# Kernel tuning notes

Measured on AMD Instinct MI355X. Metric: run time of the kernel, lower is better.

Reference implementation:

```python
import jax, jax.numpy as jnp
import numpy as np

TOP_K = 2
CAP_FACTOR = 1.25
MIN_CAPACITY = 4


def setup_inputs() -> dict:
    key = jax.random.key(0)
    k1, k2, k3, k4 = jax.random.split(key, 4)
    B, T, C, E = 8, 2048, 1024, 8
    x = jax.random.normal(k1, (B, T, C), dtype=jnp.float32)
    w_g = jax.random.normal(k2, (E, C), dtype=jnp.float32) * 0.02   # router gate (Linear, no bias)
    c_fc = jax.random.normal(k3, (E, C, 4 * C), dtype=jnp.float32) * 0.02
    c_proj = jax.random.normal(k4, (E, 4 * C, C), dtype=jnp.float32) * 0.02
    return {"x": x, "w_g": w_g, "c_fc": c_fc, "c_proj": c_proj}


def reference(x, w_g, c_fc, c_proj):
    B, T, C = x.shape
    E = w_g.shape[0]
    N = B * T
    capacity = max(MIN_CAPACITY, int(CAP_FACTOR * N * TOP_K / E))  # 5120, static

    xf = x.reshape(N, C)
    # ---- Router (eval path: no noise, no aux losses) ----
    logits = xf @ w_g.T                                   # [N, E]
    top_logits, top_idx = jax.lax.top_k(logits, TOP_K)    # [N, k]
    router_probs = jax.nn.softmax(top_logits, axis=-1)    # [N, k]

    # position in expert: cumsum over (k-major, token) flattened order
    oh = jax.nn.one_hot(top_idx, E, dtype=jnp.int32)      # [N, k, E]
    oh_t = oh.transpose(1, 0, 2).reshape(TOP_K * N, E)
    pos = jnp.cumsum(oh_t, axis=0).reshape(TOP_K, N, E).transpose(1, 0, 2)  # [N, k, E]
    rank = jnp.sum((pos - 1) * oh, axis=-1)               # [N, k], 0-based slot in expert buffer
    valid = rank < capacity                               # capacity mask
    probs_masked = router_probs * valid.astype(router_probs.dtype)
    rank_c = jnp.clip(rank, 0, capacity - 1)

    # ---- Dispatch: scatter tokens into [E, capacity, C] buffers ----
    contrib = xf[:, None, :] * valid[..., None].astype(xf.dtype)  # [N, k, C]
    buf = jnp.zeros((E, capacity, C), dtype=xf.dtype).at[top_idx, rank_c].add(contrib)

    # ---- Experts: bmm -> ReLU^2 -> bmm ----
    h = jnp.einsum('ecd,edf->ecf', buf, c_fc)             # [E, cap, 4C]
    h = jnp.square(jax.nn.relu(h))
    expert_out = jnp.einsum('ecf,efd->ecd', h, c_proj)    # [E, cap, C]

    # ---- Combine: gather expert outputs back, weight by router probs ----
    gathered = expert_out[top_idx, rank_c]                # [N, k, C]
    out = jnp.sum(gathered * probs_masked[..., None], axis=1)
    return out.reshape(B, T, C)
```

## Files before the change

### kernel.cpp

```cpp
#include <hip/hip_runtime.h>

#define NE 8
#define CAP 5120
#define NT 16384
#define CD 1024
#define FCD 4096

typedef __attribute__((ext_vector_type(8))) short short8;
typedef __attribute__((ext_vector_type(4))) float f32x4;

__device__ __forceinline__ unsigned short f2bf(float f) {
  unsigned int u = __builtin_bit_cast(unsigned int, f);
  u += 0x7FFFu + ((u >> 16) & 1u);
  return (unsigned short)(u >> 16);
}
__device__ __forceinline__ float bf2f(unsigned short u) {
  unsigned int v = ((unsigned int)u) << 16;
  return __builtin_bit_cast(float, v);
}
__device__ __forceinline__ void g2lds16(const unsigned short* g, unsigned short* l) {
  __builtin_amdgcn_global_load_lds(
      (const __attribute__((address_space(1))) unsigned int*)(unsigned long long)g,
      (__attribute__((address_space(3))) unsigned int*)l,
      16, 0, 0);
}

__global__ __launch_bounds__(256) void fill_i32_k(int* __restrict__ p, int v, int n) {
  int i = blockIdx.x * 256 + threadIdx.x;
  if (i < n) p[i] = v;
}
__global__ __launch_bounds__(256) void fill_zero_f32x4_k(float4* __restrict__ p, size_t n4) {
  size_t i = (size_t)blockIdx.x * 256 + threadIdx.x;
  if (i < n4) p[i] = make_float4(0.f, 0.f, 0.f, 0.f);
}

__global__ __launch_bounds__(256) void transpose_bf16_k(
    const float* __restrict__ in, unsigned short* __restrict__ out, int R, int Cc) {
  __shared__ float tile[64][65];
  const size_t esz = (size_t)R * Cc;
  const float* inp = in + (size_t)blockIdx.z * esz;
  unsigned short* outp = out + (size_t)blockIdx.z * esz;
  const int cbase = blockIdx.x * 64, rbase = blockIdx.y * 64;
  const int t = threadIdx.x;
#pragma unroll
  for (int i = 0; i < 4; ++i) {
    int idx = i * 256 + t;
    int r = idx >> 4, c4 = (idx & 15) * 4;
    const float4 v = *reinterpret_cast<const float4*>(inp + (size_t)(rbase + r) * Cc + cbase + c4);
    tile[r][c4 + 0] = v.x; tile[r][c4 + 1] = v.y; tile[r][c4 + 2] = v.z; tile[r][c4 + 3] = v.w;
  }
  __syncthreads();
#pragma unroll
  for (int i = 0; i < 4; ++i) {
    int idx = i * 256 + t;
    int oc = idx >> 4, q = (idx & 15) * 4;
    ushort4 o;
    o.x = f2bf(tile[q + 0][oc]); o.y = f2bf(tile[q + 1][oc]);
    o.z = f2bf(tile[q + 2][oc]); o.w = f2bf(tile[q + 3][oc]);
    *reinterpret_cast<ushort4*>(outp + (size_t)(cbase + oc) * R + rbase + q) = o;
  }
}

__global__ __launch_bounds__(256) void router_k(
    const float* __restrict__ x, const float* __restrict__ wg,
    unsigned short* __restrict__ xb, int* __restrict__ topidx, float* __restrict__ probs) {
  __shared__ float wls[NE * CD];
  const int t = threadIdx.x;
  {
    const float4* w4 = (const float4*)wg;
    float4* l4 = (float4*)wls;
    for (int i = t; i < NE * CD / 4; i += 256) l4[i] = w4[i];
  }
  __syncthreads();
  const int wave = t >> 6, lane = t & 63;
  const int gw = blockIdx.x * 4 + wave;
  const float4* wls4 = (const float4*)wls;
#pragma unroll
  for (int it = 0; it < 2; ++it) {
    const int n = gw * 2 + it;
    const float4* xr4 = (const float4*)(x + (size_t)n * CD);
    ushort4* xb4 = (ushort4*)(xb + (size_t)n * CD);
    double acc[NE] = {0, 0, 0, 0, 0, 0, 0, 0};
#pragma unroll
    for (int j = 0; j < 4; ++j) {
      const int idx = j * 64 + lane;
      const float4 xv = xr4[idx];
      ushort4 o;
      o.x = f2bf(xv.x); o.y = f2bf(xv.y); o.z = f2bf(xv.z); o.w = f2bf(xv.w);
      xb4[idx] = o;
#pragma unroll
      for (int e = 0; e < NE; ++e) {
        const float4 wv = wls4[e * 256 + idx];
        acc[e] += (double)xv.x * (double)wv.x + (double)xv.y * (double)wv.y
                + (double)xv.z * (double)wv.z + (double)xv.w * (double)wv.w;
      }
    }
#pragma unroll
    for (int s = 32; s >= 1; s >>= 1) {
#pragma unroll
      for (int e = 0; e < NE; ++e) acc[e] += __shfl_xor(acc[e], s, 64);
    }
    if (lane == 0) {
      int i1 = 0; double v1 = acc[0];
      for (int e = 1; e < NE; ++e) if (acc[e] > v1) { v1 = acc[e]; i1 = e; }
      int i2 = -1; double v2 = -1e300;
      for (int e = 0; e < NE; ++e) if (e != i1 && acc[e] > v2) { v2 = acc[e]; i2 = e; }
      float p0 = 1.0f / (1.0f + expf((float)(v2 - v1)));
      topidx[n * 2 + 0] = i1; topidx[n * 2 + 1] = i2;
      probs[n * 2 + 0] = p0; probs[n * 2 + 1] = 1.0f - p0;
    }
  }
}

__global__ __launch_bounds__(256) void hist_k(const int* __restrict__ topidx, int* __restrict__ blkhist) {
  __shared__ int h[16];
  const int t = threadIdx.x;
  if (t < 16) h[t] = 0;
  __syncthreads();
  const int n = blockIdx.x * 256 + t;
  atomicAdd(&h[topidx[n * 2 + 0]], 1);
  atomicAdd(&h[8 + topidx[n * 2 + 1]], 1);
  __syncthreads();
  if (t < 16) blkhist[blockIdx.x * 16 + t] = h[t];
}

__global__ void scan_k(const int* __restrict__ blkhist, int* __restrict__ blkoff, int* __restrict__ totals_cnt) {
  const int t = threadIdx.x;
  if (t < 16) {
    int s = 0;
    for (int b = 0; b < 64; ++b) { blkoff[b * 16 + t] = s; s += blkhist[b * 16 + t]; }
    totals_cnt[t] = s;
  }
  __syncthreads();
  if (t < 8) {
    int tot = totals_cnt[t] + totals_cnt[8 + t];
    totals_cnt[16 + t] = tot < CAP ? tot : CAP;
  }
}

__global__ __launch_bounds__(256) void rank_k(
    const int* __restrict__ topidx, const int* __restrict__ blkoff,
    const int* __restrict__ totals_cnt, int* __restrict__ ranks, int* __restrict__ slotmap) {
  __shared__ int wcnt[2][4][8];
  __shared__ int woff[2][4][8];
  const int t = threadIdx.x, wave = t >> 6, lane = t & 63;
  const int n = blockIdx.x * 256 + t;
  const int e1 = topidx[n * 2 + 0], e2 = topidx[n * 2 + 1];
  const unsigned long long lt = (1ull << lane) - 1ull;
  int pre1 = 0, pre2 = 0;
#pragma unroll
  for (int e = 0; e < 8; ++e) {
    unsigned long long m1 = __ballot(e1 == e);
    unsigned long long m2 = __ballot(e2 == e);
    if (e1 == e) pre1 = __popcll(m1 & lt);
    if (e2 == e) pre2 = __popcll(m2 & lt);
    if (lane == 0) { wcnt[0][wave][e] = __popcll(m1); wcnt[1][wave][e] = __popcll(m2); }
  }
  __syncthreads();
  if (t < 16) {
    int k = t >> 3, e = t & 7, s = 0;
    for (int w = 0; w < 4; ++w) { woff[k][w][e] = s; s += wcnt[k][w][e]; }
  }
  __syncthreads();
  int r1 = blkoff[blockIdx.x * 16 + e1] + woff[0][wave][e1] + pre1;
  int r2 = totals_cnt[e2] + blkoff[blockIdx.x * 16 + 8 + e2] + woff[1][wave][e2] + pre2;
  ranks[n * 2 + 0] = (r1 < CAP) ? r1 : -1;
  ranks[n * 2 + 1] = (r2 < CAP) ? r2 : -1;
  if (r1 < CAP) slotmap[e1 * CAP + r1] = n * 2 + 0;
  if (r2 < CAP) slotmap[e2 * CAP + r2] = n * 2 + 1;
}

template <int BM, int KDIM, int NDIM, bool GATHER, bool RELU2>
__global__ __launch_bounds__(512) void gemm8_k(
    const unsigned short* __restrict__ A, const unsigned short* __restrict__ Bt,
    unsigned short* __restrict__ Out, const int* __restrict__ slotmap,
    const int* __restrict__ cnt, int e_base) {
  constexpr int KT = KDIM / 32;
  constexpr int TM = CAP / BM;
  constexpr int TN = NDIM / 256;
  constexpr int M_REP = BM / 32;
  constexpr int MH = M_REP / 2;
  constexpr int ALOADS = BM / 128;
  constexpr int VWAIT = ALOADS + 2;

  __shared__ unsigned short lA[3][BM * 32];
  __shared__ unsigned short lB[3][256 * 32];

  const int nwg = gridDim.x;
  const int q = nwg >> 3, r = nwg & 7;
  const int xcd = blockIdx.x & 7, lin = blockIdx.x >> 3;
  const int wg = (xcd < r ? xcd * (q + 1) : r * (q + 1) + (xcd - r) * q) + lin;
  const int le = wg / (TM * TN);
  const int rem = wg % (TM * TN);
  const int nt = rem / TM;
  const int mt = rem % TM;
  const int e = e_base + le;
  if (mt * BM >= cnt[e]) return;

  const int tid = threadIdx.x;
  const int wave = tid >> 6, lane = tid & 63;
  const int wr = wave >> 2, wc = wave & 3;
  const int l15 = lane & 15, l4 = lane >> 4;

  const unsigned short* pA[ALOADS];
  const unsigned short* pB[2];
#pragma unroll
  for (int j = 0; j < ALOADS; ++j) {
    const int ci = j * 512 + tid;
    const int row = ci >> 2, cst = ci & 3;
    const int csrc = cst ^ (row & 3);
    size_t grow;
    if (GATHER) {
      const int sv = slotmap[e * CAP + mt * BM + row];
      grow = (size_t)(sv < 0 ? 0 : (sv >> 1));
    } else {
      grow = (size_t)le * CAP + mt * BM + row;
    }
    pA[j] = A + grow * KDIM + csrc * 8;
  }
#pragma unroll
  for (int j = 0; j < 2; ++j) {
    const int ci = j * 512 + tid;
    const int row = ci >> 2, cst = ci & 3;
    const int csrc = cst ^ (row & 3);
    pB[j] = Bt + ((size_t)le * NDIM + nt * 256 + row) * KDIM + csrc * 8;
  }

  int aOff[M_REP], bOff[4];
#pragma unroll
  for (int m = 0; m < M_REP; ++m)
    aOff[m] = (wr * (BM / 2) + m * 16 + l15) * 32 + ((l4 ^ (l15 & 3)) * 8);
#pragma unroll
  for (int n = 0; n < 4; ++n)
    bOff[n] = (wc * 64 + n * 16 + l15) * 32 + ((l4 ^ (l15 & 3)) * 8);

  f32x4 acc[M_REP][4] = {};

#pragma unroll
  for (int kt = 0; kt < 2; ++kt) {
#pragma unroll
    for (int j = 0; j < ALOADS; ++j)
      g2lds16(pA[j] + kt * 32, &lA[kt][(j * 512 + wave * 64) * 8]);
#pragma unroll
    for (int j = 0; j < 2; ++j)
      g2lds16(pB[j] + kt * 32, &lB[kt][(j * 512 + wave * 64) * 8]);
  }

  for (int t = 0; t < KT; ++t) {
    if (t < KT - 1) {
      if constexpr (VWAIT == 4) asm volatile("s_waitcnt vmcnt(4)" ::: "memory");
      else                      asm volatile("s_waitcnt vmcnt(3)" ::: "memory");
    } else {
      asm volatile("s_waitcnt vmcnt(0)" ::: "memory");
    }
    __builtin_amdgcn_s_barrier();
    asm volatile("" ::: "memory");

    const int s = t % 3, s2 = (t + 2) % 3;
    const unsigned short* sA = &lA[s][0];
    const unsigned short* sB = &lB[s][0];
    const bool pf = (t + 2 < KT);

    short8 aF[MH], bF[4];
#pragma unroll
    for (int m = 0; m < MH; ++m) aF[m] = *(const short8*)(sA + aOff[m]);
#pragma unroll
    for (int n = 0; n < 4; ++n) bF[n] = *(const short8*)(sB + bOff[n]);
    if (pf) {
#pragma unroll
      for (int j = 0; j < ALOADS; ++j)
        g2lds16(pA[j] + (t + 2) * 32, &lA[s2][(j * 512 + wave * 64) * 8]);
    }
    asm volatile("s_waitcnt lgkmcnt(0)" ::: "memory");
    __builtin_amdgcn_sched_barrier(0);
    __builtin_amdgcn_s_setprio(1);
#pragma unroll
    for (int m = 0; m < MH; ++m)
#pragma unroll
      for (int n = 0; n < 4; ++n)
        acc[m][n] = __builtin_amdgcn_mfma_f32_16x16x32_bf16(aF[m], bF[n], acc[m][n], 0, 0, 0);
    __builtin_amdgcn_s_setprio(0);

    short8 aG[MH];
#pragma unroll
    for (int m = 0; m < MH; ++m) aG[m] = *(const short8*)(sA + aOff[MH + m]);
    if (pf) {
#pragma unroll
      for (int j = 0; j < 2; ++j)
        g2lds16(pB[j] + (t + 2) * 32, &lB[s2][(j * 512 + wave * 64) * 8]);
    }
    asm volatile("s_waitcnt lgkmcnt(0)" ::: "memory");
    __builtin_amdgcn_sched_barrier(0);
    __builtin_amdgcn_s_setprio(1);
#pragma unroll
    for (int m = 0; m < MH; ++m)
#pragma unroll
      for (int n = 0; n < 4; ++n)
        acc[MH + m][n] = __builtin_amdgcn_mfma_f32_16x16x32_bf16(aG[m], bF[n], acc[MH + m][n], 0, 0, 0);
    __builtin_amdgcn_s_setprio(0);
  }

  const size_t rowb = (size_t)le * CAP + mt * BM + wr * (BM / 2);
  const int colb = nt * 256 + wc * 64;
#pragma unroll
  for (int m = 0; m < M_REP; ++m)
#pragma unroll
    for (int n = 0; n < 4; ++n)
#pragma unroll
      for (int rr = 0; rr < 4; ++rr) {
        float v = acc[m][n][rr];
        if (RELU2) { v = fmaxf(v, 0.0f); v = v * v; }
        Out[(rowb + m * 16 + l4 * 4 + rr) * NDIM + colb + n * 16 + l15] = f2bf(v);
      }
}

__global__ __launch_bounds__(256) void combine_k(
    const unsigned short* __restrict__ eo, const int* __restrict__ topidx,
    const float* __restrict__ probs, const int* __restrict__ ranks, float* __restrict__ out) {
  const int n = blockIdx.x, t = threadIdx.x;
  const int c = t * 4;
  const int e1 = topidx[n * 2 + 0], e2 = topidx[n * 2 + 1];
  const int r1 = ranks[n * 2 + 0], r2 = ranks[n * 2 + 1];
  const float p1 = probs[n * 2 + 0], p2 = probs[n * 2 + 1];
  float o0 = 0.f, o1 = 0.f, o2 = 0.f, o3 = 0.f;
  if (r1 >= 0) {
    const ushort4 v = *(const ushort4*)(eo + ((size_t)e1 * CAP + r1) * CD + c);
    o0 += p1 * bf2f(v.x); o1 += p1 * bf2f(v.y); o2 += p1 * bf2f(v.z); o3 += p1 * bf2f(v.w);
  }
  if (r2 >= 0) {
    const ushort4 v = *(const ushort4*)(eo + ((size_t)e2 * CAP + r2) * CD + c);
    o0 += p2 * bf2f(v.x); o1 += p2 * bf2f(v.y); o2 += p2 * bf2f(v.z); o3 += p2 * bf2f(v.w);
  }
  float4 o; o.x = o0; o.y = o1; o.z = o2; o.w = o3;
  *reinterpret_cast<float4*>(out + (size_t)n * CD + c) = o;
}

extern "C" void kernel_launch(void* const* d_in, const int* in_sizes, int n_in,
                              void* d_out, int out_size, void* d_ws, size_t ws_size,
                              hipStream_t stream) {
  const float* x = (const float*)d_in[0];
  const float* wg = (const float*)d_in[1];
  const float* cfc = (const float*)d_in[2];
  const float* cproj = (const float*)d_in[3];
  float* out = (float*)d_out;
  char* ws = (char*)d_ws;
  (void)in_sizes; (void)n_in; (void)out_size;

  const size_t W1SZ = (size_t)FCD * CD * 2;
  const size_t HSZ  = (size_t)CAP * FCD * 2;
  const size_t EOSZ = (size_t)CAP * CD * 2;

  size_t off = 0;
  auto alloc = [&](size_t bytes) { size_t o = off; off = (off + bytes + 255) & ~(size_t)255; return o; };
  unsigned short* XB = (unsigned short*)(ws + alloc((size_t)NT * CD * 2));
  int* TOPIDX  = (int*)(ws + alloc((size_t)NT * 2 * 4));
  float* PROBS = (float*)(ws + alloc((size_t)NT * 2 * 4));
  int* RANKS   = (int*)(ws + alloc((size_t)NT * 2 * 4));
  int* SLOTMAP = (int*)(ws + alloc((size_t)NE * CAP * 4));
  int* BLKHIST = (int*)(ws + alloc(64 * 16 * 4));
  int* BLKOFF  = (int*)(ws + alloc(64 * 16 * 4));
  int* TOTALS  = (int*)(ws + alloc(256));
  const size_t shared_end = off;
  int* CNT = TOTALS + 16;

  size_t woff = shared_end;
  auto walloc = [&](size_t bytes) { size_t o = woff; woff = (woff + bytes + 255) & ~(size_t)255; return o; };
  const size_t oCFCT   = walloc(NE * W1SZ);
  const size_t oCPROJT = walloc(NE * W1SZ);
  const size_t weights_end = woff;

  int EG = 0;
  for (int g = 8; g >= 1; g >>= 1) {
    size_t need = weights_end + NE * EOSZ + 512 + (size_t)g * HSZ + 512;
    if (ws_size >= need) { EG = g; break; }
  }
  if (EG == 0) {
    fill_zero_f32x4_k<<<(NT * CD / 4 + 255) / 256, 256, 0, stream>>>((float4*)out, (size_t)NT * CD / 4);
    return;
  }

  fill_i32_k<<<(NE * CAP + 255) / 256, 256, 0, stream>>>(SLOTMAP, -1, NE * CAP);
  router_k<<<2048, 256, 0, stream>>>(x, wg, XB, TOPIDX, PROBS);
  hist_k<<<64, 256, 0, stream>>>(TOPIDX, BLKHIST);
  scan_k<<<1, 64, 0, stream>>>(BLKHIST, BLKOFF, TOTALS);
  rank_k<<<64, 256, 0, stream>>>(TOPIDX, BLKOFF, TOTALS, RANKS, SLOTMAP);

  unsigned short* CFCT   = (unsigned short*)(ws + oCFCT);
  unsigned short* CPROJT = (unsigned short*)(ws + oCPROJT);
  transpose_bf16_k<<<dim3(FCD / 64, CD / 64, NE), 256, 0, stream>>>(cfc, CFCT, CD, FCD);
  transpose_bf16_k<<<dim3(CD / 64, FCD / 64, NE), 256, 0, stream>>>(cproj, CPROJT, FCD, CD);

  size_t eoff = weights_end;
  auto ealloc = [&](size_t bytes) { size_t o = eoff; eoff = (eoff + bytes + 255) & ~(size_t)255; return o; };
  unsigned short* EO = (unsigned short*)(ws + ealloc(NE * EOSZ));
  unsigned short* H  = (unsigned short*)(ws + ealloc((size_t)EG * HSZ));

  for (int g = 0; g < NE / EG; ++g) {
    const int eb = g * EG;
    gemm8_k<256, CD, FCD, true, true><<<EG * (CAP / 256) * (FCD / 256), 512, 0, stream>>>(
        XB, CFCT + (size_t)eb * FCD * CD, H, SLOTMAP, CNT, eb);
    gemm8_k<128, FCD, CD, false, false><<<EG * (CAP / 128) * (CD / 256), 512, 0, stream>>>(
        H, CPROJT + (size_t)eb * CD * FCD, EO + (size_t)eb * CAP * CD, SLOTMAP, CNT, eb);
  }
  combine_k<<<NT, 256, 0, stream>>>(EO, TOPIDX, PROBS, RANKS, out);
}
```

Measured before the change: 993.3 us.

## Generalize GEMM wave/tile shape and use 128x128 tiles for down-projection

Makes the expert GEMM kernel generic over the wave grid (WM x WN) and the N tile size. The second GEMM (down-projection, K=4096) now runs as 128x128 tiles on 4 waves instead of 128x256 on 8 waves, doubling its grid size, presumably so more workgroups are available for the CUs. It also changes the LDS XOR swizzle from row&3 to (row>>1)&3, aiming to reduce bank conflicts on the fragment reads. Smaller tiles reduce data reuse per workgroup and raise global traffic for the B operand.

```diff
diff --git a/kernel.cpp b/kernel.cpp
--- a/kernel.cpp
+++ b/kernel.cpp
@@ -170,21 +170,24 @@
   if (r2 < CAP) slotmap[e2 * CAP + r2] = n * 2 + 1;
 }
 
-template <int BM, int KDIM, int NDIM, bool GATHER, bool RELU2>
-__global__ __launch_bounds__(512) void gemm8_k(
+template <int WM, int WN, int BM, int BN, int KDIM, int NDIM, bool GATHER, bool RELU2>
+__global__ __launch_bounds__(WM * WN * 64) void gemm8_k(
     const unsigned short* __restrict__ A, const unsigned short* __restrict__ Bt,
     unsigned short* __restrict__ Out, const int* __restrict__ slotmap,
     const int* __restrict__ cnt, int e_base) {
+  constexpr int THREADS = WM * WN * 64;
   constexpr int KT = KDIM / 32;
   constexpr int TM = CAP / BM;
-  constexpr int TN = NDIM / 256;
-  constexpr int M_REP = BM / 32;
+  constexpr int TN = NDIM / BN;
+  constexpr int M_REP = BM / WM / 16;
+  constexpr int N_REP = BN / WN / 16;
   constexpr int MH = M_REP / 2;
-  constexpr int ALOADS = BM / 128;
-  constexpr int VWAIT = ALOADS + 2;
+  constexpr int ALOADS = BM * 4 / THREADS;
+  constexpr int BLOADS = BN * 4 / THREADS;
+  static_assert(ALOADS + BLOADS == 4, "vmcnt literal assumes 4 loads/wave/tile");
 
   __shared__ unsigned short lA[3][BM * 32];
-  __shared__ unsigned short lB[3][256 * 32];
+  __shared__ unsigned short lB[3][BN * 32];
 
   const int nwg = gridDim.x;
   const int q = nwg >> 3, r = nwg & 7;
@@ -199,16 +202,16 @@
 
   const int tid = threadIdx.x;
   const int wave = tid >> 6, lane = tid & 63;
-  const int wr = wave >> 2, wc = wave & 3;
+  const int wr = wave / WN, wc = wave % WN;
   const int l15 = lane & 15, l4 = lane >> 4;
 
   const unsigned short* pA[ALOADS];
-  const unsigned short* pB[2];
+  const unsigned short* pB[BLOADS];
 #pragma unroll
   for (int j = 0; j < ALOADS; ++j) {
-    const int ci = j * 512 + tid;
+    const int ci = j * THREADS + tid;
     const int row = ci >> 2, cst = ci & 3;
-    const int csrc = cst ^ (row & 3);
+    const int csrc = cst ^ ((row >> 1) & 3);
     size_t grow;
     if (GATHER) {
       const int sv = slotmap[e * CAP + mt * BM + row];
@@ -219,40 +222,37 @@
     pA[j] = A + grow * KDIM + csrc * 8;
   }
 #pragma unroll
-  for (int j = 0; j < 2; ++j) {
-    const int ci = j * 512 + tid;
+  for (int j = 0; j < BLOADS; ++j) {
+    const int ci = j * THREADS + tid;
     const int row = ci >> 2, cst = ci & 3;
-    const int csrc = cst ^ (row & 3);
-    pB[j] = Bt + ((size_t)le * NDIM + nt * 256 + row) * KDIM + csrc * 8;
-  }
-
-  int aOff[M_REP], bOff[4];
+    const int csrc = cst ^ ((row >> 1) & 3);
+    pB[j] = Bt + ((size_t)le * NDIM + nt * BN + row) * KDIM + csrc * 8;
+  }
+
+  const int ksw = (l4 ^ ((l15 >> 1) & 3)) * 8;
+  int aOff[M_REP], bOff[N_REP];
 #pragma unroll
   for (int m = 0; m < M_REP; ++m)
-    aOff[m] = (wr * (BM / 2) + m * 16 + l15) * 32 + ((l4 ^ (l15 & 3)) * 8);
-#pragma unroll
-  for (int n = 0; n < 4; ++n)
-    bOff[n] = (wc * 64 + n * 16 + l15) * 32 + ((l4 ^ (l15 & 3)) * 8);
-
-  f32x4 acc[M_REP][4] = {};
+    aOff[m] = (wr * (BM / WM) + m * 16 + l15) * 32 + ksw;
+#pragma unroll
+  for (int n = 0; n < N_REP; ++n)
+    bOff[n] = (wc * (BN / WN) + n * 16 + l15) * 32 + ksw;
+
+  f32x4 acc[M_REP][N_REP] = {};
 
 #pragma unroll
   for (int kt = 0; kt < 2; ++kt) {
 #pragma unroll
     for (int j = 0; j < ALOADS; ++j)
-      g2lds16(pA[j] + kt * 32, &lA[kt][(j * 512 + wave * 64) * 8]);
-#pragma unroll
-    for (int j = 0; j < 2; ++j)
-      g2lds16(pB[j] + kt * 32, &lB[kt][(j * 512 + wave * 64) * 8]);
+      g2lds16(pA[j] + kt * 32, &lA[kt][(j * THREADS + wave * 64) * 8]);
+#pragma unroll
+    for (int j = 0; j < BLOADS; ++j)
+      g2lds16(pB[j] + kt * 32, &lB[kt][(j * THREADS + wave * 64) * 8]);
   }
 
   for (int t = 0; t < KT; ++t) {
-    if (t < KT - 1) {
-      if constexpr (VWAIT == 4) asm volatile("s_waitcnt vmcnt(4)" ::: "memory");
-      else                      asm volatile("s_waitcnt vmcnt(3)" ::: "memory");
-    } else {
-      asm volatile("s_waitcnt vmcnt(0)" ::: "memory");
-    }
+    if (t < KT - 1) asm volatile("s_waitcnt vmcnt(4)" ::: "memory");
+    else            asm volatile("s_waitcnt vmcnt(0)" ::: "memory");
     __builtin_amdgcn_s_barrier();
     asm volatile("" ::: "memory");
 
@@ -261,15 +261,15 @@
     const unsigned short* sB = &lB[s][0];
     const bool pf = (t + 2 < KT);
 
-    short8 aF[MH], bF[4];
+    short8 aF[MH], bF[N_REP];
 #pragma unroll
     for (int m = 0; m < MH; ++m) aF[m] = *(const short8*)(sA + aOff[m]);
 #pragma unroll
-    for (int n = 0; n < 4; ++n) bF[n] = *(const short8*)(sB + bOff[n]);
+    for (int n = 0; n < N_REP; ++n) bF[n] = *(const short8*)(sB + bOff[n]);
     if (pf) {
 #pragma unroll
       for (int j = 0; j < ALOADS; ++j)
-        g2lds16(pA[j] + (t + 2) * 32, &lA[s2][(j * 512 + wave * 64) * 8]);
+        g2lds16(pA[j] + (t + 2) * 32, &lA[s2][(j * THREADS + wave * 64) * 8]);
     }
     asm volatile("s_waitcnt lgkmcnt(0)" ::: "memory");
     __builtin_amdgcn_sched_barrier(0);
@@ -277,7 +277,7 @@
 #pragma unroll
     for (int m = 0; m < MH; ++m)
 #pragma unroll
-      for (int n = 0; n < 4; ++n)
+      for (int n = 0; n < N_REP; ++n)
         acc[m][n] = __builtin_amdgcn_mfma_f32_16x16x32_bf16(aF[m], bF[n], acc[m][n], 0, 0, 0);
     __builtin_amdgcn_s_setprio(0);
 
@@ -286,8 +286,8 @@
     for (int m = 0; m < MH; ++m) aG[m] = *(const short8*)(sA + aOff[MH + m]);
     if (pf) {
 #pragma unroll
-      for (int j = 0; j < 2; ++j)
-        g2lds16(pB[j] + (t + 2) * 32, &lB[s2][(j * 512 + wave * 64) * 8]);
+      for (int j = 0; j < BLOADS; ++j)
+        g2lds16(pB[j] + (t + 2) * 32, &lB[s2][(j * THREADS + wave * 64) * 8]);
     }
     asm volatile("s_waitcnt lgkmcnt(0)" ::: "memory");
     __builtin_amdgcn_sched_barrier(0);
@@ -295,17 +295,17 @@
 #pragma unroll
     for (int m = 0; m < MH; ++m)
 #pragma unroll
-      for (int n = 0; n < 4; ++n)
+      for (int n = 0; n < N_REP; ++n)
         acc[MH + m][n] = __builtin_amdgcn_mfma_f32_16x16x32_bf16(aG[m], bF[n], acc[MH + m][n], 0, 0, 0);
     __builtin_amdgcn_s_setprio(0);
   }
 
-  const size_t rowb = (size_t)le * CAP + mt * BM + wr * (BM / 2);
-  const int colb = nt * 256 + wc * 64;
+  const size_t rowb = (size_t)le * CAP + mt * BM + wr * (BM / WM);
+  const int colb = nt * BN + wc * (BN / WN);
 #pragma unroll
   for (int m = 0; m < M_REP; ++m)
 #pragma unroll
-    for (int n = 0; n < 4; ++n)
+    for (int n = 0; n < N_REP; ++n)
 #pragma unroll
       for (int rr = 0; rr < 4; ++rr) {
         float v = acc[m][n][rr];
@@ -397,9 +397,11 @@
 
   for (int g = 0; g < NE / EG; ++g) {
     const int eb = g * EG;
-    gemm8_k<256, CD, FCD, true, true><<<EG * (CAP / 256) * (FCD / 256), 512, 0, stream>>>(
+    gemm8_k<2, 4, 256, 256, CD, FCD, true, true>
+        <<<EG * (CAP / 256) * (FCD / 256), 512, 0, stream>>>(
         XB, CFCT + (size_t)eb * FCD * CD, H, SLOTMAP, CNT, eb);
-    gemm8_k<128, FCD, CD, false, false><<<EG * (CAP / 128) * (CD / 256), 512, 0, stream>>>(
+    gemm8_k<2, 2, 128, 128, FCD, CD, false, false>
+        <<<EG * (CAP / 128) * (CD / 128), 256, 0, stream>>>(
         H, CPROJT + (size_t)eb * CD * FCD, EO + (size_t)eb * CAP * CD, SLOTMAP, CNT, eb);
   }
   combine_k<<<NT, 256, 0, stream>>>(EO, TOPIDX, PROBS, RANKS, out);
```

Result: no change. 993.1 us (-0.0%).

## Restructure expert GEMM into K=64 double-buffered ping-pong quadrant pipeline

Applied to the files above, without the earlier changes.

Replaces the triple-buffered K=32 GEMM mainloop with a double-buffered K=64 tile. Each iteration is split into four quadrant MFMA phases, with the global-to-LDS loads for the next tile interleaved between them and barriers placed between phases. The LDS swizzle changes to an 8-chunk XOR pattern and the wave-to-output mapping is reorganized into quadrants. The goal is fewer barriers per K step and better overlap of loads with MFMA work. The cost is more complex wait-count bookkeeping and a changed LDS footprint that could affect occupancy.

```diff
diff --git a/kernel.cpp b/kernel.cpp
--- a/kernel.cpp
+++ b/kernel.cpp
@@ -171,20 +171,22 @@
 }
 
 template <int BM, int KDIM, int NDIM, bool GATHER, bool RELU2>
-__global__ __launch_bounds__(512) void gemm8_k(
+__global__ __launch_bounds__(512) void gemm8p_k(
     const unsigned short* __restrict__ A, const unsigned short* __restrict__ Bt,
     unsigned short* __restrict__ Out, const int* __restrict__ slotmap,
     const int* __restrict__ cnt, int e_base) {
-  constexpr int KT = KDIM / 32;
+  constexpr int BN = 256;
+  constexpr int KT = KDIM / 64;
   constexpr int TM = CAP / BM;
-  constexpr int TN = NDIM / 256;
+  constexpr int TN = NDIM / BN;
   constexpr int M_REP = BM / 32;
-  constexpr int MH = M_REP / 2;
-  constexpr int ALOADS = BM / 128;
-  constexpr int VWAIT = ALOADS + 2;
-
-  __shared__ unsigned short lA[3][BM * 32];
-  __shared__ unsigned short lB[3][256 * 32];
+  constexpr int QM = M_REP / 2;
+  constexpr int AL = BM / 128;
+  constexpr int BL = 2;
+  constexpr int V = AL + BL;
+
+  __shared__ unsigned short lA[2][BM * 64];
+  __shared__ unsigned short lB[2][BN * 64];
 
   const int nwg = gridDim.x;
   const int q = nwg >> 3, r = nwg & 7;
@@ -202,116 +204,137 @@
   const int wr = wave >> 2, wc = wave & 3;
   const int l15 = lane & 15, l4 = lane >> 4;
 
-  const unsigned short* pA[ALOADS];
-  const unsigned short* pB[2];
-#pragma unroll
-  for (int j = 0; j < ALOADS; ++j) {
-    const int ci = j * 512 + tid;
-    const int row = ci >> 2, cst = ci & 3;
-    const int csrc = cst ^ (row & 3);
-    size_t grow;
-    if (GATHER) {
-      const int sv = slotmap[e * CAP + mt * BM + row];
-      grow = (size_t)(sv < 0 ? 0 : (sv >> 1));
-    } else {
-      grow = (size_t)le * CAP + mt * BM + row;
-    }
-    pA[j] = A + grow * KDIM + csrc * 8;
-  }
-#pragma unroll
-  for (int j = 0; j < 2; ++j) {
-    const int ci = j * 512 + tid;
-    const int row = ci >> 2, cst = ci & 3;
-    const int csrc = cst ^ (row & 3);
-    pB[j] = Bt + ((size_t)le * NDIM + nt * 256 + row) * KDIM + csrc * 8;
-  }
-
-  int aOff[M_REP], bOff[4];
-#pragma unroll
-  for (int m = 0; m < M_REP; ++m)
-    aOff[m] = (wr * (BM / 2) + m * 16 + l15) * 32 + ((l4 ^ (l15 & 3)) * 8);
-#pragma unroll
-  for (int n = 0; n < 4; ++n)
-    bOff[n] = (wc * 64 + n * 16 + l15) * 32 + ((l4 ^ (l15 & 3)) * 8);
+  const unsigned short* sApt[2][AL];
+  const unsigned short* sBpt[2][BL];
+#pragma unroll
+  for (int h = 0; h < 2; ++h) {
+#pragma unroll
+    for (int j = 0; j < AL; ++j) {
+      const int lc = j * 512 + tid;
+      const int lr = lc >> 3, pc = lc & 7;
+      const int logc = pc ^ (lr & 7);
+      const int rowT = h * (BM / 2) + lr;
+      size_t grow;
+      if (GATHER) {
+        const int sv = slotmap[e * CAP + mt * BM + rowT];
+        grow = (size_t)(sv < 0 ? 0 : (sv >> 1));
+      } else {
+        grow = (size_t)le * CAP + mt * BM + rowT;
+      }
+      sApt[h][j] = A + grow * KDIM + logc * 8;
+    }
+#pragma unroll
+    for (int j = 0; j < BL; ++j) {
+      const int lc = j * 512 + tid;
+      const int lr = lc >> 3, pc = lc & 7;
+      const int logc = pc ^ (lr & 7);
+      sBpt[h][j] = Bt + ((size_t)le * NDIM + nt * BN + h * 128 + lr) * KDIM + logc * 8;
+    }
+  }
+
+#define STAGE_A(sl, h, tt)                                                              \
+  do { _Pragma("unroll") for (int j = 0; j < AL; ++j)                                   \
+    g2lds16(sApt[h][j] + (size_t)(tt) * 64,                                             \
+            &lA[sl][((h) * (BM / 2) * 8 + j * 512 + wave * 64) * 8]); } while (0)
+#define STAGE_B(sl, h, tt)                                                              \
+  do { _Pragma("unroll") for (int j = 0; j < BL; ++j)                                   \
+    g2lds16(sBpt[h][j] + (size_t)(tt) * 64,                                             \
+            &lB[sl][((h) * 128 * 8 + j * 512 + wave * 64) * 8]); } while (0)
+
+  const int kidx0 = ((0 * 4 + l4) ^ (l15 & 7)) * 8;
+  const int kidx1 = ((1 * 4 + l4) ^ (l15 & 7)) * 8;
+
+#define RD_A(mh)                                                                        \
+  do { _Pragma("unroll") for (int m = 0; m < QM; ++m) {                                 \
+    const int row = (mh) * (BM / 2) + wr * (BM / 4) + m * 16 + l15;                     \
+    aF[m][0] = *(const short8*)(bA + row * 64 + kidx0);                                 \
+    aF[m][1] = *(const short8*)(bA + row * 64 + kidx1); } } while (0)
+#define RD_B(nh)                                                                        \
+  do { _Pragma("unroll") for (int n = 0; n < 2; ++n) {                                  \
+    const int row = (nh) * 128 + wc * 32 + n * 16 + l15;                                \
+    bF[n][0] = *(const short8*)(bB + row * 64 + kidx0);                                 \
+    bF[n][1] = *(const short8*)(bB + row * 64 + kidx1); } } while (0)
+#define LGK0()                                                                          \
+  do { asm volatile("s_waitcnt lgkmcnt(0)" ::: "memory");                               \
+       __builtin_amdgcn_sched_barrier(0); } while (0)
+#define MF(mh, nh)                                                                      \
+  do { __builtin_amdgcn_s_setprio(1);                                                   \
+    _Pragma("unroll") for (int m = 0; m < QM; ++m)                                      \
+      _Pragma("unroll") for (int n = 0; n < 2; ++n) {                                   \
+        acc[(mh) * QM + m][(nh) * 2 + n] = __builtin_amdgcn_mfma_f32_16x16x32_bf16(     \
+            aF[m][0], bF[n][0], acc[(mh) * QM + m][(nh) * 2 + n], 0, 0, 0);             \
+        acc[(mh) * QM + m][(nh) * 2 + n] = __builtin_amdgcn_mfma_f32_16x16x32_bf16(     \
+            aF[m][1], bF[n][1], acc[(mh) * QM + m][(nh) * 2 + n], 0, 0, 0); }           \
+    __builtin_amdgcn_s_setprio(0); } while (0)
+#define VMC_V()  do { if constexpr (V == 4) asm volatile("s_waitcnt vmcnt(4)" ::: "memory"); \
+                      else asm volatile("s_waitcnt vmcnt(3)" ::: "memory"); } while (0)
+#define VMC_2()  asm volatile("s_waitcnt vmcnt(2)" ::: "memory")
+#define VMC_0()  asm volatile("s_waitcnt vmcnt(0)" ::: "memory")
+#define BAR()    do { __builtin_amdgcn_s_barrier(); asm volatile("" ::: "memory"); } while (0)
 
   f32x4 acc[M_REP][4] = {};
-
-#pragma unroll
-  for (int kt = 0; kt < 2; ++kt) {
-#pragma unroll
-    for (int j = 0; j < ALOADS; ++j)
-      g2lds16(pA[j] + kt * 32, &lA[kt][(j * 512 + wave * 64) * 8]);
-#pragma unroll
-    for (int j = 0; j < 2; ++j)
-      g2lds16(pB[j] + kt * 32, &lB[kt][(j * 512 + wave * 64) * 8]);
-  }
-
+  short8 aF[QM][2], bF[2][2];
+
+  STAGE_A(0, 0, 0); STAGE_B(0, 0, 0); STAGE_A(0, 1, 0); STAGE_B(0, 1, 0);
+  VMC_V();
+  BAR();
+
+  int s = 0;
   for (int t = 0; t < KT; ++t) {
-    if (t < KT - 1) {
-      if constexpr (VWAIT == 4) asm volatile("s_waitcnt vmcnt(4)" ::: "memory");
-      else                      asm volatile("s_waitcnt vmcnt(3)" ::: "memory");
-    } else {
-      asm volatile("s_waitcnt vmcnt(0)" ::: "memory");
-    }
-    __builtin_amdgcn_s_barrier();
-    asm volatile("" ::: "memory");
-
-    const int s = t % 3, s2 = (t + 2) % 3;
-    const unsigned short* sA = &lA[s][0];
-    const unsigned short* sB = &lB[s][0];
-    const bool pf = (t + 2 < KT);
-
-    short8 aF[MH], bF[4];
-#pragma unroll
-    for (int m = 0; m < MH; ++m) aF[m] = *(const short8*)(sA + aOff[m]);
-#pragma unroll
-    for (int n = 0; n < 4; ++n) bF[n] = *(const short8*)(sB + bOff[n]);
-    if (pf) {
-#pragma unroll
-      for (int j = 0; j < ALOADS; ++j)
-        g2lds16(pA[j] + (t + 2) * 32, &lA[s2][(j * 512 + wave * 64) * 8]);
-    }
-    asm volatile("s_waitcnt lgkmcnt(0)" ::: "memory");
-    __builtin_amdgcn_sched_barrier(0);
-    __builtin_amdgcn_s_setprio(1);
-#pragma unroll
-    for (int m = 0; m < MH; ++m)
-#pragma unroll
-      for (int n = 0; n < 4; ++n)
-        acc[m][n] = __builtin_amdgcn_mfma_f32_16x16x32_bf16(aF[m], bF[n], acc[m][n], 0, 0, 0);
-    __builtin_amdgcn_s_setprio(0);
-
-    short8 aG[MH];
-#pragma unroll
-    for (int m = 0; m < MH; ++m) aG[m] = *(const short8*)(sA + aOff[MH + m]);
-    if (pf) {
-#pragma unroll
-      for (int j = 0; j < 2; ++j)
-        g2lds16(pB[j] + (t + 2) * 32, &lB[s2][(j * 512 + wave * 64) * 8]);
-    }
-    asm volatile("s_waitcnt lgkmcnt(0)" ::: "memory");
-    __builtin_amdgcn_sched_barrier(0);
-    __builtin_amdgcn_s_setprio(1);
-#pragma unroll
-    for (int m = 0; m < MH; ++m)
-#pragma unroll
-      for (int n = 0; n < 4; ++n)
-        acc[MH + m][n] = __builtin_amdgcn_mfma_f32_16x16x32_bf16(aG[m], bF[n], acc[MH + m][n], 0, 0, 0);
-    __builtin_amdgcn_s_setprio(0);
-  }
-
-  const size_t rowb = (size_t)le * CAP + mt * BM + wr * (BM / 2);
-  const int colb = nt * 256 + wc * 64;
-#pragma unroll
-  for (int m = 0; m < M_REP; ++m)
-#pragma unroll
-    for (int n = 0; n < 4; ++n)
+    const int s2 = s ^ 1;
+    const unsigned short* bA = &lA[s][0];
+    const unsigned short* bB = &lB[s][0];
+    const bool more = (t + 1 < KT);
+
+    RD_A(0); RD_B(0);
+    if (more) { STAGE_A(s2, 0, t + 1); VMC_V(); } else { VMC_2(); }
+    LGK0();
+    MF(0, 0);
+    BAR();
+    RD_A(1);
+    if (more) { STAGE_B(s2, 0, t + 1); VMC_V(); } else { VMC_0(); }
+    LGK0();
+    MF(1, 0);
+    BAR();
+    RD_B(1);
+    if (more) STAGE_A(s2, 1, t + 1);
+    LGK0();
+    MF(1, 1);
+    RD_A(0);
+    if (more) { STAGE_B(s2, 1, t + 1); VMC_V(); }
+    LGK0();
+    MF(0, 1);
+    if (more) BAR();
+    s = s2;
+  }
+
+  const size_t rowb = (size_t)le * CAP + mt * BM;
+  const int colb = nt * BN;
+#pragma unroll
+  for (int i = 0; i < M_REP; ++i) {
+    const int mh = i / QM, m = i % QM;
+#pragma unroll
+    for (int j = 0; j < 4; ++j) {
+      const int nh = j / 2, n = j % 2;
 #pragma unroll
       for (int rr = 0; rr < 4; ++rr) {
-        float v = acc[m][n][rr];
+        float v = acc[i][j][rr];
         if (RELU2) { v = fmaxf(v, 0.0f); v = v * v; }
-        Out[(rowb + m * 16 + l4 * 4 + rr) * NDIM + colb + n * 16 + l15] = f2bf(v);
+        const size_t orow = rowb + mh * (BM / 2) + wr * (BM / 4) + m * 16 + l4 * 4 + rr;
+        Out[orow * NDIM + colb + nh * 128 + wc * 32 + n * 16 + l15] = f2bf(v);
       }
+    }
+  }
+#undef STAGE_A
+#undef STAGE_B
+#undef RD_A
+#undef RD_B
+#undef LGK0
+#undef MF
+#undef VMC_V
+#undef VMC_2
+#undef VMC_0
+#undef BAR
 }
 
 __global__ __launch_bounds__(256) void combine_k(
@@ -397,9 +420,11 @@
 
   for (int g = 0; g < NE / EG; ++g) {
     const int eb = g * EG;
-    gemm8_k<256, CD, FCD, true, true><<<EG * (CAP / 256) * (FCD / 256), 512, 0, stream>>>(
+    gemm8p_k<256, CD, FCD, true, true>
+        <<<EG * (CAP / 256) * (FCD / 256), 512, 0, stream>>>(
         XB, CFCT + (size_t)eb * FCD * CD, H, SLOTMAP, CNT, eb);
-    gemm8_k<128, FCD, CD, false, false><<<EG * (CAP / 128) * (CD / 256), 512, 0, stream>>>(
+    gemm8p_k<128, FCD, CD, false, false>
+        <<<EG * (CAP / 128) * (CD / 256), 512, 0, stream>>>(
         H, CPROJT + (size_t)eb * CD * FCD, EO + (size_t)eb * CAP * CD, SLOTMAP, CNT, eb);
   }
   combine_k<<<NT, 256, 0, stream>>>(EO, TOPIDX, PROBS, RANKS, out);
```

New measurement: 1.123 ms. 13.1% more time.

## Replace pipelined 512-thread expert GEMM with simple single-buffer 256x128 tile kernel

Applied to the files above, without the earlier changes.

Swaps the triple-buffered, software-pipelined 512-thread GEMM for a simpler 256-thread kernel with a fixed 256x128 tile, a single LDS buffer and two block barriers per K step. It also drops the XCD-aware block remapping in favour of m-major block ordering, changes the LDS swizzle pattern and requests two workgroups per CU. The intent is to gain occupancy and simpler scheduling, but it gives up the overlap of global loads with MFMA work and the per-XCD locality.

```diff
diff --git a/kernel.cpp b/kernel.cpp
--- a/kernel.cpp
+++ b/kernel.cpp
@@ -170,45 +170,38 @@
   if (r2 < CAP) slotmap[e2 * CAP + r2] = n * 2 + 1;
 }
 
-template <int BM, int KDIM, int NDIM, bool GATHER, bool RELU2>
-__global__ __launch_bounds__(512) void gemm8_k(
+template <int KDIM, int NDIM, bool GATHER, bool RELU2>
+__global__ __launch_bounds__(256, 2) void gemm_m97b_k(
     const unsigned short* __restrict__ A, const unsigned short* __restrict__ Bt,
     unsigned short* __restrict__ Out, const int* __restrict__ slotmap,
-    const int* __restrict__ cnt, int e_base) {
+    const int* __restrict__ cnt, int e_base, int n_le) {
+  constexpr int BM = 256, BN = 128;
   constexpr int KT = KDIM / 32;
-  constexpr int TM = CAP / BM;
-  constexpr int TN = NDIM / 256;
-  constexpr int M_REP = BM / 32;
-  constexpr int MH = M_REP / 2;
-  constexpr int ALOADS = BM / 128;
-  constexpr int VWAIT = ALOADS + 2;
-
-  __shared__ unsigned short lA[3][BM * 32];
-  __shared__ unsigned short lB[3][256 * 32];
-
-  const int nwg = gridDim.x;
-  const int q = nwg >> 3, r = nwg & 7;
-  const int xcd = blockIdx.x & 7, lin = blockIdx.x >> 3;
-  const int wg = (xcd < r ? xcd * (q + 1) : r * (q + 1) + (xcd - r) * q) + lin;
-  const int le = wg / (TM * TN);
-  const int rem = wg % (TM * TN);
-  const int nt = rem / TM;
-  const int mt = rem % TM;
+  constexpr int TN = NDIM / BN;
+
+  __shared__ unsigned short lA[BM * 32];
+  __shared__ unsigned short lB[BN * 32];
+
+  const int ent = n_le * TN;
+  const int mt = blockIdx.x / ent;
+  const int rem = blockIdx.x % ent;
+  const int le = rem / TN;
+  const int nt = rem % TN;
   const int e = e_base + le;
   if (mt * BM >= cnt[e]) return;
 
   const int tid = threadIdx.x;
   const int wave = tid >> 6, lane = tid & 63;
-  const int wr = wave >> 2, wc = wave & 3;
+  const int wr = wave >> 1, wc = wave & 1;
   const int l15 = lane & 15, l4 = lane >> 4;
 
-  const unsigned short* pA[ALOADS];
+  const unsigned short* pA[4];
   const unsigned short* pB[2];
 #pragma unroll
-  for (int j = 0; j < ALOADS; ++j) {
-    const int ci = j * 512 + tid;
+  for (int j = 0; j < 4; ++j) {
+    const int ci = j * 256 + tid;
     const int row = ci >> 2, cst = ci & 3;
-    const int csrc = cst ^ (row & 3);
+    const int csrc = cst ^ ((row >> 1) & 3);
     size_t grow;
     if (GATHER) {
       const int sv = slotmap[e * CAP + mt * BM + row];
@@ -220,90 +213,42 @@
   }
 #pragma unroll
   for (int j = 0; j < 2; ++j) {
-    const int ci = j * 512 + tid;
+    const int ci = j * 256 + tid;
     const int row = ci >> 2, cst = ci & 3;
-    const int csrc = cst ^ (row & 3);
-    pB[j] = Bt + ((size_t)le * NDIM + nt * 256 + row) * KDIM + csrc * 8;
-  }
-
-  int aOff[M_REP], bOff[4];
-#pragma unroll
-  for (int m = 0; m < M_REP; ++m)
-    aOff[m] = (wr * (BM / 2) + m * 16 + l15) * 32 + ((l4 ^ (l15 & 3)) * 8);
-#pragma unroll
-  for (int n = 0; n < 4; ++n)
-    bOff[n] = (wc * 64 + n * 16 + l15) * 32 + ((l4 ^ (l15 & 3)) * 8);
-
-  f32x4 acc[M_REP][4] = {};
-
-#pragma unroll
-  for (int kt = 0; kt < 2; ++kt) {
-#pragma unroll
-    for (int j = 0; j < ALOADS; ++j)
-      g2lds16(pA[j] + kt * 32, &lA[kt][(j * 512 + wave * 64) * 8]);
-#pragma unroll
-    for (int j = 0; j < 2; ++j)
-      g2lds16(pB[j] + kt * 32, &lB[kt][(j * 512 + wave * 64) * 8]);
-  }
+    const int csrc = cst ^ ((row >> 1) & 3);
+    pB[j] = Bt + ((size_t)le * NDIM + nt * BN + row) * KDIM + csrc * 8;
+  }
+
+  const int ksw = (l4 ^ ((l15 >> 1) & 3)) * 8;
+
+  f32x4 acc[8][4] = {};
 
   for (int t = 0; t < KT; ++t) {
-    if (t < KT - 1) {
-      if constexpr (VWAIT == 4) asm volatile("s_waitcnt vmcnt(4)" ::: "memory");
-      else                      asm volatile("s_waitcnt vmcnt(3)" ::: "memory");
-    } else {
-      asm volatile("s_waitcnt vmcnt(0)" ::: "memory");
-    }
-    __builtin_amdgcn_s_barrier();
-    asm volatile("" ::: "memory");
-
-    const int s = t % 3, s2 = (t + 2) % 3;
-    const unsigned short* sA = &lA[s][0];
-    const unsigned short* sB = &lB[s][0];
-    const bool pf = (t + 2 < KT);
-
-    short8 aF[MH], bF[4];
-#pragma unroll
-    for (int m = 0; m < MH; ++m) aF[m] = *(const short8*)(sA + aOff[m]);
-#pragma unroll
-    for (int n = 0; n < 4; ++n) bF[n] = *(const short8*)(sB + bOff[n]);
-    if (pf) {
-#pragma unroll
-      for (int j = 0; j < ALOADS; ++j)
-        g2lds16(pA[j] + (t + 2) * 32, &lA[s2][(j * 512 + wave * 64) * 8]);
-    }
-    asm volatile("s_waitcnt lgkmcnt(0)" ::: "memory");
-    __builtin_amdgcn_sched_barrier(0);
-    __builtin_amdgcn_s_setprio(1);
-#pragma unroll
-    for (int m = 0; m < MH; ++m)
+    __syncthreads();
+#pragma unroll
+    for (int j = 0; j < 4; ++j) g2lds16(pA[j] + (size_t)t * 32, &lA[(j * 256 + wave * 64) * 8]);
+#pragma unroll
+    for (int j = 0; j < 2; ++j) g2lds16(pB[j] + (size_t)t * 32, &lB[(j * 256 + wave * 64) * 8]);
+    __syncthreads();
+
+    short8 aF[8], bF[4];
+#pragma unroll
+    for (int m = 0; m < 8; ++m)
+      aF[m] = *(const short8*)(&lA[(wr * 128 + m * 16 + l15) * 32 + ksw]);
+#pragma unroll
+    for (int n = 0; n < 4; ++n)
+      bF[n] = *(const short8*)(&lB[(wc * 64 + n * 16 + l15) * 32 + ksw]);
+#pragma unroll
+    for (int m = 0; m < 8; ++m)
 #pragma unroll
       for (int n = 0; n < 4; ++n)
         acc[m][n] = __builtin_amdgcn_mfma_f32_16x16x32_bf16(aF[m], bF[n], acc[m][n], 0, 0, 0);
-    __builtin_amdgcn_s_setprio(0);
-
-    short8 aG[MH];
-#pragma unroll
-    for (int m = 0; m < MH; ++m) aG[m] = *(const short8*)(sA + aOff[MH + m]);
-    if (pf) {
-#pragma unroll
-      for (int j = 0; j < 2; ++j)
-        g2lds16(pB[j] + (t + 2) * 32, &lB[s2][(j * 512 + wave * 64) * 8]);
-    }
-    asm volatile("s_waitcnt lgkmcnt(0)" ::: "memory");
-    __builtin_amdgcn_sched_barrier(0);
-    __builtin_amdgcn_s_setprio(1);
-#pragma unroll
-    for (int m = 0; m < MH; ++m)
-#pragma unroll
-      for (int n = 0; n < 4; ++n)
-        acc[MH + m][n] = __builtin_amdgcn_mfma_f32_16x16x32_bf16(aG[m], bF[n], acc[MH + m][n], 0, 0, 0);
-    __builtin_amdgcn_s_setprio(0);
-  }
-
-  const size_t rowb = (size_t)le * CAP + mt * BM + wr * (BM / 2);
-  const int colb = nt * 256 + wc * 64;
-#pragma unroll
-  for (int m = 0; m < M_REP; ++m)
+  }
+
+  const size_t rowb = (size_t)le * CAP + mt * BM + wr * 128;
+  const int colb = nt * BN + wc * 64;
+#pragma unroll
+  for (int m = 0; m < 8; ++m)
 #pragma unroll
     for (int n = 0; n < 4; ++n)
 #pragma unroll
@@ -397,10 +342,12 @@
 
   for (int g = 0; g < NE / EG; ++g) {
     const int eb = g * EG;
-    gemm8_k<256, CD, FCD, true, true><<<EG * (CAP / 256) * (FCD / 256), 512, 0, stream>>>(
-        XB, CFCT + (size_t)eb * FCD * CD, H, SLOTMAP, CNT, eb);
-    gemm8_k<128, FCD, CD, false, false><<<EG * (CAP / 128) * (CD / 256), 512, 0, stream>>>(
-        H, CPROJT + (size_t)eb * CD * FCD, EO + (size_t)eb * CAP * CD, SLOTMAP, CNT, eb);
+    gemm_m97b_k<CD, FCD, true, true>
+        <<<EG * (CAP / 256) * (FCD / 128), 256, 0, stream>>>(
+        XB, CFCT + (size_t)eb * FCD * CD, H, SLOTMAP, CNT, eb, EG);
+    gemm_m97b_k<FCD, CD, false, false>
+        <<<EG * (CAP / 256) * (CD / 128), 256, 0, stream>>>(
+        H, CPROJT + (size_t)eb * CD * FCD, EO + (size_t)eb * CAP * CD, SLOTMAP, CNT, eb, EG);
   }
   combine_k<<<NT, 256, 0, stream>>>(EO, TOPIDX, PROBS, RANKS, out);
 }
```

After: 1.299 ms. 30.8% more time.
